# Optimization experiments

Hardware: AMD Instinct MI355X
Metric: run time of the kernel (lower is better)

Reference implementation:

```python
import jax, jax.numpy as jnp
import numpy as np

NQ = 8          # n_qubits
NC = 4          # n_cycles of the angle encoder
PI = np.float32(np.pi)
LAYER_QUBITS = [[0, 1, 2, 3, 4, 5, 6, 7], [1, 3, 5, 7]]  # active qubits per conv layer
FINAL_QUBITS = [3, 7]                                    # active after last pooling
CX = jnp.array([[1, 0, 0, 0], [0, 1, 0, 0], [0, 0, 0, 1], [0, 0, 1, 0]], jnp.complex64)


def apply1(psi, U, q):
    """Apply 1-qubit gate U ((2,2) shared or (B,2,2) batched) on qubit q. psi: (B,2,...,2)."""
    psi = jnp.moveaxis(psi, 1 + q, -1)
    if U.ndim == 3:
        psi = jnp.einsum('bij,b...j->b...i', U, psi)
    else:
        psi = jnp.einsum('ij,...j->...i', U, psi)
    return jnp.moveaxis(psi, -1, 1 + q)


def apply2(psi, U, q0, q1):
    """Apply 2-qubit gate U (4,4) on (q0,q1); q0 is the more-significant wire."""
    psi = jnp.moveaxis(psi, (1 + q0, 1 + q1), (-2, -1))
    sh = psi.shape
    psi = jnp.einsum('ij,...j->...i', U, psi.reshape(sh[:-2] + (4,)))
    return jnp.moveaxis(psi.reshape(sh), (-2, -1), (1 + q0, 1 + q1))


def rz_mat(t):
    return jnp.array([[jnp.exp(-0.5j * t), 0.0], [0.0, jnp.exp(0.5j * t)]]).astype(jnp.complex64)


def ry_mat(t):
    c, s = jnp.cos(t / 2), jnp.sin(t / 2)
    return jnp.array([[c, -s], [s, c]]).astype(jnp.complex64)


def crx_mat(t):
    c = jnp.cos(t / 2).astype(jnp.complex64)
    s = jnp.sin(t / 2).astype(jnp.complex64)
    M = jnp.eye(4, dtype=jnp.complex64)
    return M.at[2, 2].set(c).at[3, 3].set(c).at[2, 3].set(-1j * s).at[3, 2].set(-1j * s)


def u3_mat(t, p, l):
    c, s = jnp.cos(t / 2), jnp.sin(t / 2)
    return jnp.array([[c + 0j, -jnp.exp(1j * l) * s],
                      [jnp.exp(1j * p) * s, jnp.exp(1j * (p + l)) * c]]).astype(jnp.complex64)


def expz(psi, q):
    """<Z_q> = P(q=0) - P(q=1)."""
    p = psi.real ** 2 + psi.imag ** 2
    p = jnp.moveaxis(p, 1 + q, 1).reshape(p.shape[0], 2, -1).sum(-1)
    return p[:, 0] - p[:, 1]


def encode(x):
    """Angle-encoding circuit (circuit_builder): NC cycles of RY(x) + CNOT ring."""
    B = x.shape[0]
    psi = jnp.zeros((B, 2 ** NQ), jnp.complex64).at[:, 0].set(1.0).reshape((B,) + (2,) * NQ)
    for c in range(NC):
        ang = x[:, c * NQ:(c + 1) * NQ]
        cc, ss = jnp.cos(ang / 2), jnp.sin(ang / 2)
        for q in range(NQ):
            U = jnp.stack([jnp.stack([cc[:, q], -ss[:, q]], -1),
                           jnp.stack([ss[:, q], cc[:, q]], -1)], -2).astype(jnp.complex64)
            psi = apply1(psi, U, q)
        for q in range(NQ):
            psi = apply2(psi, CX, q, (q + 1) % NQ)
    return psi


def forward(x, rz_p, ry_p, ry2_p, crx_p, u3_p, u3b_p, W1, b1, W2, b2):
    psi0 = encode(x)
    psi1 = psi0  # deepcopy of encoded state for the second feature map
    for layer in range(2):
        aq = LAYER_QUBITS[layer]
        n = len(aq)
        RZp, RYp, RY2p = rz_mat(rz_p[layer]), ry_mat(ry_p[layer]), ry_mat(ry2_p[layer])
        RZm, RZpl = rz_mat(-PI / 2), rz_mat(PI / 2)
        # circuit 1: ZNOTY-style conv blocks, even pairs then odd pairs
        for parity in (0, 1):
            for i in range(parity, n - 1, 2):
                qc, qt = aq[i], aq[i + 1]
                psi0 = apply1(psi0, RZm, qt)
                psi0 = apply2(psi0, CX, qt, qc)
                psi0 = apply1(psi0, RZp, qc)
                psi0 = apply1(psi0, RYp, qt)
                psi0 = apply2(psi0, CX, qc, qt)
                psi0 = apply1(psi0, RY2p, qt)
                psi0 = apply2(psi0, CX, qt, qc)
                psi0 = apply1(psi0, RZpl, qc)
        remain = [aq[i] for i in range(n) if i % 2 == 1]
        U3a = u3_mat(u3_p[layer, 0], u3_p[layer, 1], u3_p[layer, 2])
        for q in remain:
            psi0 = apply1(psi0, U3a, q)
        # circuit 2: CRX conv blocks, even pairs then odd pairs
        CRXp = crx_mat(crx_p[layer])
        for parity in (0, 1):
            for i in range(parity, n - 1, 2):
                psi1 = apply2(psi1, CRXp, aq[i], aq[i + 1])
        U3b = u3_mat(u3b_p[layer, 0], u3b_p[layer, 1], u3b_p[layer, 2])
        for q in remain:
            psi1 = apply1(psi1, U3b, q)
    xv = jnp.stack([expz(psi0, q) for q in FINAL_QUBITS], 1)  # (B,2)
    yv = jnp.stack([expz(psi1, q) for q in FINAL_QUBITS], 1)  # (B,2)
    feat = jnp.concatenate([xv, yv], 1)                       # (B,4)
    h = jnp.tanh(feat @ W1.T + b1)
    return jax.nn.sigmoid(h @ W2.T + b2)


def setup_inputs() -> dict:
    key = jax.random.key(0)
    ks = jax.random.split(key, 12)
    B = 8192
    return {
        'x': jax.random.normal(ks[0], (B, NC * NQ), jnp.float32),
        'rz_p': jax.random.normal(ks[1], (2,), jnp.float32) * 0.5,
        'ry_p': jax.random.normal(ks[2], (2,), jnp.float32) * 0.5,
        'ry2_p': jax.random.normal(ks[3], (2,), jnp.float32) * 0.5,
        'crx_p': jax.random.normal(ks[4], (2,), jnp.float32) * 0.5,
        'u3_p': jax.random.normal(ks[5], (2, 3), jnp.float32) * 0.5,
        'u3b_p': jax.random.normal(ks[6], (2, 3), jnp.float32) * 0.5,
        'W1': jax.random.normal(ks[7], (15, 4), jnp.float32) * 0.4,
        'b1': jax.random.normal(ks[8], (15,), jnp.float32) * 0.1,
        'W2': jax.random.normal(ks[9], (1, 15), jnp.float32) * 0.25,
        'b2': jax.random.normal(ks[10], (1,), jnp.float32) * 0.1,
    }


def reference(x, rz_p, ry_p, ry2_p, crx_p, u3_p, u3b_p, W1, b1, W2, b2):
    return forward(x, rz_p, ry_p, ry2_p, crx_p, u3_p, u3b_p, W1, b1, W2, b2)
```

## Files before the change

kernel.cpp:

```cpp
#include <hip/hip_runtime.h>

#define DEV __device__ __forceinline__

struct C2 { float r, i; };


template<int P>
DEV void ry_cross(float* pr, float* pi, float gc, float gs, int lane) {
  const float cb = ((lane >> P) & 1) ? gs : -gs;
  #pragma unroll
  for (int s = 0; s < 4; ++s) {
    float br = __shfl_xor(pr[s], 1 << P);
    float bi = __shfl_xor(pi[s], 1 << P);
    pr[s] = gc * pr[s] + cb * br;
    pi[s] = gc * pi[s] + cb * bi;
  }
}

template<int M>
DEV void ry_in(float* pr, float* pi, float gc, float gs) {
  #pragma unroll
  for (int s = 0; s < 4; ++s) if (!(s & M)) {
    const int s1 = s | M;
    float ar = pr[s], ai = pi[s], br = pr[s1], bi = pi[s1];
    pr[s]  = gc * ar - gs * br;  pi[s]  = gc * ai - gs * bi;
    pr[s1] = gs * ar + gc * br;  pi[s1] = gs * ai + gc * bi;
  }
}

template<int PC, int PT>
DEV void cx_cc(float* pr, float* pi, int lane) {
  const bool h = (lane >> PC) & 1;
  #pragma unroll
  for (int s = 0; s < 4; ++s) {
    float tr = __shfl_xor(pr[s], 1 << PT);
    float ti = __shfl_xor(pi[s], 1 << PT);
    pr[s] = h ? tr : pr[s];
    pi[s] = h ? ti : pi[s];
  }
}

template<int PC, int MT>
DEV void cx_ci(float* pr, float* pi, int lane) {
  const bool h = (lane >> PC) & 1;
  #pragma unroll
  for (int s = 0; s < 4; ++s) if (!(s & MT)) {
    const int s1 = s | MT;
    float ar = pr[s], br = pr[s1];
    pr[s] = h ? br : ar;  pr[s1] = h ? ar : br;
    float ai = pi[s], bi = pi[s1];
    pi[s] = h ? bi : ai;  pi[s1] = h ? ai : bi;
  }
}

template<int MC, int MT>
DEV void cx_ii(float* pr, float* pi) {
  #pragma unroll
  for (int s = 0; s < 4; ++s) if ((s & MC) && !(s & MT)) {
    const int s1 = s | MT;
    float t;
    t = pr[s]; pr[s] = pr[s1]; pr[s1] = t;
    t = pi[s]; pi[s] = pi[s1]; pi[s1] = t;
  }
}

template<int MC, int PT>
DEV void cx_ic(float* pr, float* pi) {
  #pragma unroll
  for (int s = 0; s < 4; ++s) if (s & MC) {
    pr[s] = __shfl_xor(pr[s], 1 << PT);
    pi[s] = __shfl_xor(pi[s], 1 << PT);
  }
}


template<int PC, int PT>
DEV void u4_cc(float* pr, float* pi, const float* cw, int lay, int lane) {
  const int r = (((lane >> PC) & 1) << 1) | ((lane >> PT) & 1);
  const int base = (lay * 16 + r * 4) * 2;
  const float w0r = cw[base + (r ^ 0) * 2], w0i = cw[base + (r ^ 0) * 2 + 1];
  const float w1r = cw[base + (r ^ 1) * 2], w1i = cw[base + (r ^ 1) * 2 + 1];
  const float w2r = cw[base + (r ^ 2) * 2], w2i = cw[base + (r ^ 2) * 2 + 1];
  const float w3r = cw[base + (r ^ 3) * 2], w3i = cw[base + (r ^ 3) * 2 + 1];
  #pragma unroll
  for (int s = 0; s < 4; ++s) {
    float ar = pr[s], ai = pi[s];
    float tr = __shfl_xor(ar, 1 << PT),               ti = __shfl_xor(ai, 1 << PT);
    float cr = __shfl_xor(ar, 1 << PC),               ci = __shfl_xor(ai, 1 << PC);
    float ur = __shfl_xor(ar, (1 << PC) | (1 << PT)), ui = __shfl_xor(ai, (1 << PC) | (1 << PT));
    pr[s] = w0r*ar - w0i*ai + w1r*tr - w1i*ti + w2r*cr - w2i*ci + w3r*ur - w3i*ui;
    pi[s] = w0r*ai + w0i*ar + w1r*ti + w1i*tr + w2r*ci + w2i*cr + w3r*ui + w3i*ur;
  }
}

template<int PC, int MT>
DEV void u4_ci(float* pr, float* pi, const float* cw, int lay, int lane) {
  const int bc = (lane >> PC) & 1;
  const int r0 = bc << 1, r1 = r0 | 1;
  const int b0 = (lay * 16 + r0 * 4) * 2;
  const int b1 = (lay * 16 + r1 * 4) * 2;
  const float A0r = cw[b0 + (r0 ^ 0) * 2], A0i = cw[b0 + (r0 ^ 0) * 2 + 1];
  const float A1r = cw[b0 + (r0 ^ 1) * 2], A1i = cw[b0 + (r0 ^ 1) * 2 + 1];
  const float A2r = cw[b0 + (r0 ^ 2) * 2], A2i = cw[b0 + (r0 ^ 2) * 2 + 1];
  const float A3r = cw[b0 + (r0 ^ 3) * 2], A3i = cw[b0 + (r0 ^ 3) * 2 + 1];
  const float B0r = cw[b1 + (r1 ^ 0) * 2], B0i = cw[b1 + (r1 ^ 0) * 2 + 1];
  const float B1r = cw[b1 + (r1 ^ 1) * 2], B1i = cw[b1 + (r1 ^ 1) * 2 + 1];
  const float B2r = cw[b1 + (r1 ^ 2) * 2], B2i = cw[b1 + (r1 ^ 2) * 2 + 1];
  const float B3r = cw[b1 + (r1 ^ 3) * 2], B3i = cw[b1 + (r1 ^ 3) * 2 + 1];
  #pragma unroll
  for (int s = 0; s < 4; ++s) if (!(s & MT)) {
    const int s1 = s | MT;
    float ar = pr[s], ai = pi[s], br = pr[s1], bi = pi[s1];
    float xar = __shfl_xor(ar, 1 << PC), xai = __shfl_xor(ai, 1 << PC);
    float xbr = __shfl_xor(br, 1 << PC), xbi = __shfl_xor(bi, 1 << PC);
    pr[s]  = A0r*ar - A0i*ai + A1r*br - A1i*bi + A2r*xar - A2i*xai + A3r*xbr - A3i*xbi;
    pi[s]  = A0r*ai + A0i*ar + A1r*bi + A1i*br + A2r*xai + A2i*xar + A3r*xbi + A3i*xbr;
    pr[s1] = B0r*br - B0i*bi + B1r*ar - B1i*ai + B2r*xbr - B2i*xbi + B3r*xar - B3i*xai;
    pi[s1] = B0r*bi + B0i*br + B1r*ai + B1i*ar + B2r*xbi + B2i*xbr + B3r*xai + B3i*xar;
  }
}

DEV void u4_ii_full(float* pr, float* pi, const float* cw, int lay) {
  float nr[4], ni[4];
  #pragma unroll
  for (int r = 0; r < 4; ++r) {
    float ar = 0.0f, ai = 0.0f;
    #pragma unroll
    for (int c = 0; c < 4; ++c) {
      float ur = cw[(lay * 16 + r * 4 + c) * 2];
      float ui = cw[(lay * 16 + r * 4 + c) * 2 + 1];
      ar += ur * pr[c] - ui * pi[c];
      ai += ur * pi[c] + ui * pr[c];
    }
    nr[r] = ar; ni[r] = ai;
  }
  #pragma unroll
  for (int r = 0; r < 4; ++r) { pr[r] = nr[r]; pi[r] = ni[r]; }
}


DEV void u3_make(float t, float p, float l, C2* u) {
  float c = __cosf(0.5f * t), s = __sinf(0.5f * t);
  float cp = __cosf(p), sp = __sinf(p);
  float cl = __cosf(l), sl = __sinf(l);
  float cpl = __cosf(p + l), spl = __sinf(p + l);
  u[0] = C2{c, 0.0f};
  u[1] = C2{-cl * s, -sl * s};
  u[2] = C2{cp * s, sp * s};
  u[3] = C2{cpl * c, spl * c};
}

template<int P>
DEV void u3_cross(float* pr, float* pi, const C2* u, int lane) {
  const bool h = (lane >> P) & 1;
  const float car = h ? u[3].r : u[0].r, cai = h ? u[3].i : u[0].i;
  const float cbr = h ? u[2].r : u[1].r, cbi = h ? u[2].i : u[1].i;
  #pragma unroll
  for (int s = 0; s < 4; ++s) {
    float br = __shfl_xor(pr[s], 1 << P);
    float bi = __shfl_xor(pi[s], 1 << P);
    float ar = pr[s], ai = pi[s];
    pr[s] = car*ar - cai*ai + cbr*br - cbi*bi;
    pi[s] = car*ai + cai*ar + cbr*bi + cbi*br;
  }
}

template<int M>
DEV void u3_in(float* pr, float* pi, const C2* u) {
  #pragma unroll
  for (int s = 0; s < 4; ++s) if (!(s & M)) {
    const int s1 = s | M;
    float ar = pr[s], ai = pi[s], br = pr[s1], bi = pi[s1];
    pr[s]  = u[0].r*ar - u[0].i*ai + u[1].r*br - u[1].i*bi;
    pi[s]  = u[0].r*ai + u[0].i*ar + u[1].r*bi + u[1].i*br;
    pr[s1] = u[2].r*ar - u[2].i*ai + u[3].r*br - u[3].i*bi;
    pi[s1] = u[2].r*ai + u[2].i*ar + u[3].r*bi + u[3].i*br;
  }
}


template<int PC, int PT>
DEV void crx_cc(float* pr, float* pi, float c, float s, int lane) {
  const bool h = (lane >> PC) & 1;
  const float cc = h ? c : 1.0f;
  const float ss = h ? s : 0.0f;
  #pragma unroll
  for (int k = 0; k < 4; ++k) {
    float br = __shfl_xor(pr[k], 1 << PT);
    float bi = __shfl_xor(pi[k], 1 << PT);
    float ar = pr[k], ai = pi[k];
    pr[k] = cc * ar + ss * bi;
    pi[k] = cc * ai - ss * br;
  }
}

template<int PC, int MT>
DEV void crx_ci(float* pr, float* pi, float c, float s, int lane) {
  const bool h = (lane >> PC) & 1;
  const float cc = h ? c : 1.0f;
  const float ss = h ? s : 0.0f;
  #pragma unroll
  for (int k = 0; k < 4; ++k) if (!(k & MT)) {
    const int k1 = k | MT;
    float ar = pr[k], ai = pi[k], br = pr[k1], bi = pi[k1];
    pr[k]  = cc * ar + ss * bi;
    pi[k]  = cc * ai - ss * br;
    pr[k1] = cc * br + ss * ai;
    pi[k1] = cc * bi - ss * ar;
  }
}

template<int MC, int MT>
DEV void crx_ii(float* pr, float* pi, float c, float s) {
  #pragma unroll
  for (int k = 0; k < 4; ++k) if ((k & MC) && !(k & MT)) {
    const int k1 = k | MT;
    float ar = pr[k], ai = pi[k], br = pr[k1], bi = pi[k1];
    pr[k]  = c * ar + s * bi;
    pi[k]  = c * ai - s * br;
    pr[k1] = c * br + s * ai;
    pi[k1] = c * bi - s * ar;
  }
}


DEV void expz37(const float* pr, const float* pi, int lane, float& z3, float& z7) {
  float t3 = 0.0f, t7 = 0.0f;
  #pragma unroll
  for (int s = 0; s < 4; ++s) {
    float p = pr[s] * pr[s] + pi[s] * pi[s];
    t3 += p;
    t7 += (s & 1) ? -p : p;
  }
  t3 = ((lane >> 2) & 1) ? -t3 : t3;
  #pragma unroll
  for (int m = 1; m < 64; m <<= 1) {
    t3 += __shfl_xor(t3, m);
    t7 += __shfl_xor(t7, m);
  }
  z3 = t3; z7 = t7;
}


__global__ __launch_bounds__(256, 4)
void qcnn_kernel(const float* __restrict__ x,
                 const float* __restrict__ rz_p, const float* __restrict__ ry_p,
                 const float* __restrict__ ry2_p, const float* __restrict__ crx_p,
                 const float* __restrict__ u3_p, const float* __restrict__ u3b_p,
                 const float* __restrict__ W1, const float* __restrict__ b1,
                 const float* __restrict__ W2, const float* __restrict__ b2,
                 float* __restrict__ out, int B) {
  __shared__ float cw[64];

  const int tid  = threadIdx.x;
  const int lane = tid & 63;
  const int wave = tid >> 6;
  const int elem = blockIdx.x * 4 + wave;
  const int elemc = elem < B ? elem : (B - 1);

  if (tid < 32) {
    const int lay = tid >> 4, e = tid & 15, i4 = e >> 2, j4 = e & 3;
    const int base = tid & 48;
    const float c45 = 0.70710678118654752f;
    float rz = rz_p[lay], ry = ry_p[lay], ry2 = ry2_p[lay];
    float mr = (i4 == j4) ? c45 : 0.0f;
    float mi = (i4 == j4) ? ((i4 & 1) ? -c45 : c45) : 0.0f;
    { int t = (i4 & 1) ? (i4 ^ 2) : i4; int src = base | (t << 2) | j4;
      mr = __shfl(mr, src); mi = __shfl(mi, src); }
    { float cz = __cosf(0.5f * rz), sz = __sinf(0.5f * rz);
      float di = (i4 & 2) ? sz : -sz;
      float nr = cz * mr - di * mi, ni = cz * mi + di * mr; mr = nr; mi = ni; }
    { float cy = __cosf(0.5f * ry), sy = __sinf(0.5f * ry);
      int src = base | ((i4 ^ 1) << 2) | j4;
      float orr = __shfl(mr, src), oii = __shfl(mi, src);
      float sg = (i4 & 1) ? sy : -sy;
      mr = cy * mr + sg * orr; mi = cy * mi + sg * oii; }
    { int t = (i4 & 2) ? (i4 ^ 1) : i4; int src = base | (t << 2) | j4;
      mr = __shfl(mr, src); mi = __shfl(mi, src); }
    { float cy = __cosf(0.5f * ry2), sy = __sinf(0.5f * ry2);
      int src = base | ((i4 ^ 1) << 2) | j4;
      float orr = __shfl(mr, src), oii = __shfl(mi, src);
      float sg = (i4 & 1) ? sy : -sy;
      mr = cy * mr + sg * orr; mi = cy * mi + sg * oii; }
    { int t = (i4 & 1) ? (i4 ^ 2) : i4; int src = base | (t << 2) | j4;
      mr = __shfl(mr, src); mi = __shfl(mi, src); }
    { float di = (i4 & 2) ? c45 : -c45;
      float nr = c45 * mr - di * mi, ni = c45 * mi + di * mr; mr = nr; mi = ni; }
    cw[(lay * 16 + e) * 2]     = mr;
    cw[(lay * 16 + e) * 2 + 1] = mi;
  }

  float a0 = x[(size_t)elemc * 32 + (lane & 31)];
  float ch = __cosf(0.5f * a0), sh = __sinf(0.5f * a0);

  float pr[4], pi[4];
  #pragma unroll
  for (int s = 0; s < 4; ++s) { pr[s] = 0.0f; pi[s] = 0.0f; }
  pr[0] = (lane == 0) ? 1.0f : 0.0f;

  #pragma unroll 1
  for (int c = 0; c < 4; ++c) {
    const int cb = c * 8;
    float gc, gs;
    gc = __shfl(ch, cb + 0); gs = __shfl(sh, cb + 0); ry_cross<5>(pr, pi, gc, gs, lane);
    gc = __shfl(ch, cb + 1); gs = __shfl(sh, cb + 1); ry_cross<4>(pr, pi, gc, gs, lane);
    gc = __shfl(ch, cb + 2); gs = __shfl(sh, cb + 2); ry_cross<3>(pr, pi, gc, gs, lane);
    gc = __shfl(ch, cb + 3); gs = __shfl(sh, cb + 3); ry_cross<2>(pr, pi, gc, gs, lane);
    gc = __shfl(ch, cb + 4); gs = __shfl(sh, cb + 4); ry_cross<1>(pr, pi, gc, gs, lane);
    gc = __shfl(ch, cb + 5); gs = __shfl(sh, cb + 5); ry_cross<0>(pr, pi, gc, gs, lane);
    gc = __shfl(ch, cb + 6); gs = __shfl(sh, cb + 6); ry_in<2>(pr, pi, gc, gs);
    gc = __shfl(ch, cb + 7); gs = __shfl(sh, cb + 7); ry_in<1>(pr, pi, gc, gs);
    cx_cc<5, 4>(pr, pi, lane);
    cx_cc<4, 3>(pr, pi, lane);
    cx_cc<3, 2>(pr, pi, lane);
    cx_cc<2, 1>(pr, pi, lane);
    cx_cc<1, 0>(pr, pi, lane);
    cx_ci<0, 2>(pr, pi, lane);
    cx_ii<2, 1>(pr, pi);
    cx_ic<1, 5>(pr, pi);
  }

  float qr[4], qi[4];
  #pragma unroll
  for (int s = 0; s < 4; ++s) { qr[s] = pr[s]; qi[s] = pi[s]; }

  __syncthreads();

  u4_cc<5, 4>(pr, pi, cw, 0, lane);
  u4_cc<3, 2>(pr, pi, cw, 0, lane);
  u4_cc<1, 0>(pr, pi, cw, 0, lane);
  u4_ii_full(pr, pi, cw, 0);
  u4_cc<4, 3>(pr, pi, cw, 0, lane);
  u4_cc<2, 1>(pr, pi, cw, 0, lane);
  u4_ci<0, 2>(pr, pi, cw, 0, lane);
  {
    C2 u[4]; u3_make(u3_p[0], u3_p[1], u3_p[2], u);
    u3_cross<4>(pr, pi, u, lane);
    u3_cross<2>(pr, pi, u, lane);
    u3_cross<0>(pr, pi, u, lane);
    u3_in<1>(pr, pi, u);
  }
  u4_cc<4, 2>(pr, pi, cw, 1, lane);
  u4_ci<0, 1>(pr, pi, cw, 1, lane);
  u4_cc<2, 0>(pr, pi, cw, 1, lane);
  {
    C2 u[4]; u3_make(u3_p[3], u3_p[4], u3_p[5], u);
    u3_cross<2>(pr, pi, u, lane);
    u3_in<1>(pr, pi, u);
  }

  {
    float t = crx_p[0];
    float cc = __cosf(0.5f * t), ss = __sinf(0.5f * t);
    crx_cc<5, 4>(qr, qi, cc, ss, lane);
    crx_cc<3, 2>(qr, qi, cc, ss, lane);
    crx_cc<1, 0>(qr, qi, cc, ss, lane);
    crx_ii<2, 1>(qr, qi, cc, ss);
    crx_cc<4, 3>(qr, qi, cc, ss, lane);
    crx_cc<2, 1>(qr, qi, cc, ss, lane);
    crx_ci<0, 2>(qr, qi, cc, ss, lane);
  }
  {
    C2 u[4]; u3_make(u3b_p[0], u3b_p[1], u3b_p[2], u);
    u3_cross<4>(qr, qi, u, lane);
    u3_cross<2>(qr, qi, u, lane);
    u3_cross<0>(qr, qi, u, lane);
    u3_in<1>(qr, qi, u);
  }
  {
    float t = crx_p[1];
    float cc = __cosf(0.5f * t), ss = __sinf(0.5f * t);
    crx_cc<4, 2>(qr, qi, cc, ss, lane);
    crx_ci<0, 1>(qr, qi, cc, ss, lane);
    crx_cc<2, 0>(qr, qi, cc, ss, lane);
  }
  {
    C2 u[4]; u3_make(u3b_p[3], u3b_p[4], u3b_p[5], u);
    u3_cross<2>(qr, qi, u, lane);
    u3_in<1>(qr, qi, u);
  }

  float f0, f1, f2, f3;
  expz37(pr, pi, lane, f0, f1);
  expz37(qr, qi, lane, f2, f3);

  const int sub = lane & 15;
  const int j = (sub < 15) ? sub : 0;
  float acc = W1[j * 4 + 0] * f0 + W1[j * 4 + 1] * f1 +
              W1[j * 4 + 2] * f2 + W1[j * 4 + 3] * f3 + b1[j];
  float e2 = __expf(2.0f * acc);
  float th = (e2 - 1.0f) / (e2 + 1.0f);
  float part = (sub < 15) ? th * W2[j] : 0.0f;
  #pragma unroll
  for (int m = 1; m < 16; m <<= 1) part += __shfl_xor(part, m);

  if (lane == 0 && elem < B) {
    float z = part + b2[0];
    out[elem] = 1.0f / (1.0f + __expf(-z));
  }
}

extern "C" void kernel_launch(void* const* d_in, const int* in_sizes, int n_in,
                              void* d_out, int out_size, void* d_ws, size_t ws_size,
                              hipStream_t stream) {
  (void)n_in; (void)out_size; (void)d_ws; (void)ws_size;
  const float* x     = (const float*)d_in[0];
  const float* rz_p  = (const float*)d_in[1];
  const float* ry_p  = (const float*)d_in[2];
  const float* ry2_p = (const float*)d_in[3];
  const float* crx_p = (const float*)d_in[4];
  const float* u3_p  = (const float*)d_in[5];
  const float* u3b_p = (const float*)d_in[6];
  const float* W1    = (const float*)d_in[7];
  const float* b1    = (const float*)d_in[8];
  const float* W2    = (const float*)d_in[9];
  const float* b2    = (const float*)d_in[10];
  float* out = (float*)d_out;

  const int B = in_sizes[0] / 32;
  const int blocks = (B + 3) / 4;
  qcnn_kernel<<<dim3(blocks), dim3(256), 0, stream>>>(
      x, rz_p, ry_p, ry2_p, crx_p, u3_p, u3b_p, W1, b1, W2, b2, out, B);
}
```

Measured before the change: 141.7 us.

## Map two batch elements per wave with 8 amplitudes per lane

Each wave now simulates two batch elements, one per 32-lane half, and each lane holds 8 complex amplitudes in registers instead of 4. The qubit-to-lane and qubit-to-register mapping changes to match, and the two branch circuits (u4/u3 and crx/u3b) are interleaved for more instruction-level parallelism. The aim is to halve the number of waves and turn more gates into register-local work rather than cross-lane shuffles. In exchange each lane uses more registers, which may lower occupancy.

```diff
diff --git a/kernel.cpp b/kernel.cpp
--- a/kernel.cpp
+++ b/kernel.cpp
@@ -9,7 +9,7 @@
 DEV void ry_cross(float* pr, float* pi, float gc, float gs, int lane) {
   const float cb = ((lane >> P) & 1) ? gs : -gs;
   #pragma unroll
-  for (int s = 0; s < 4; ++s) {
+  for (int s = 0; s < 8; ++s) {
     float br = __shfl_xor(pr[s], 1 << P);
     float bi = __shfl_xor(pi[s], 1 << P);
     pr[s] = gc * pr[s] + cb * br;
@@ -20,7 +20,7 @@
 template<int M>
 DEV void ry_in(float* pr, float* pi, float gc, float gs) {
   #pragma unroll
-  for (int s = 0; s < 4; ++s) if (!(s & M)) {
+  for (int s = 0; s < 8; ++s) if (!(s & M)) {
     const int s1 = s | M;
     float ar = pr[s], ai = pi[s], br = pr[s1], bi = pi[s1];
     pr[s]  = gc * ar - gs * br;  pi[s]  = gc * ai - gs * bi;
@@ -32,7 +32,7 @@
 DEV void cx_cc(float* pr, float* pi, int lane) {
   const bool h = (lane >> PC) & 1;
   #pragma unroll
-  for (int s = 0; s < 4; ++s) {
+  for (int s = 0; s < 8; ++s) {
     float tr = __shfl_xor(pr[s], 1 << PT);
     float ti = __shfl_xor(pi[s], 1 << PT);
     pr[s] = h ? tr : pr[s];
@@ -44,7 +44,7 @@
 DEV void cx_ci(float* pr, float* pi, int lane) {
   const bool h = (lane >> PC) & 1;
   #pragma unroll
-  for (int s = 0; s < 4; ++s) if (!(s & MT)) {
+  for (int s = 0; s < 8; ++s) if (!(s & MT)) {
     const int s1 = s | MT;
     float ar = pr[s], br = pr[s1];
     pr[s] = h ? br : ar;  pr[s1] = h ? ar : br;
@@ -56,7 +56,7 @@
 template<int MC, int MT>
 DEV void cx_ii(float* pr, float* pi) {
   #pragma unroll
-  for (int s = 0; s < 4; ++s) if ((s & MC) && !(s & MT)) {
+  for (int s = 0; s < 8; ++s) if ((s & MC) && !(s & MT)) {
     const int s1 = s | MT;
     float t;
     t = pr[s]; pr[s] = pr[s1]; pr[s1] = t;
@@ -67,7 +67,7 @@
 template<int MC, int PT>
 DEV void cx_ic(float* pr, float* pi) {
   #pragma unroll
-  for (int s = 0; s < 4; ++s) if (s & MC) {
+  for (int s = 0; s < 8; ++s) if (s & MC) {
     pr[s] = __shfl_xor(pr[s], 1 << PT);
     pi[s] = __shfl_xor(pi[s], 1 << PT);
   }
@@ -83,7 +83,7 @@
   const float w2r = cw[base + (r ^ 2) * 2], w2i = cw[base + (r ^ 2) * 2 + 1];
   const float w3r = cw[base + (r ^ 3) * 2], w3i = cw[base + (r ^ 3) * 2 + 1];
   #pragma unroll
-  for (int s = 0; s < 4; ++s) {
+  for (int s = 0; s < 8; ++s) {
     float ar = pr[s], ai = pi[s];
     float tr = __shfl_xor(ar, 1 << PT),               ti = __shfl_xor(ai, 1 << PT);
     float cr = __shfl_xor(ar, 1 << PC),               ci = __shfl_xor(ai, 1 << PC);
@@ -108,7 +108,7 @@
   const float B2r = cw[b1 + (r1 ^ 2) * 2], B2i = cw[b1 + (r1 ^ 2) * 2 + 1];
   const float B3r = cw[b1 + (r1 ^ 3) * 2], B3i = cw[b1 + (r1 ^ 3) * 2 + 1];
   #pragma unroll
-  for (int s = 0; s < 4; ++s) if (!(s & MT)) {
+  for (int s = 0; s < 8; ++s) if (!(s & MT)) {
     const int s1 = s | MT;
     float ar = pr[s], ai = pi[s], br = pr[s1], bi = pi[s1];
     float xar = __shfl_xor(ar, 1 << PC), xai = __shfl_xor(ai, 1 << PC);
@@ -120,22 +120,25 @@
   }
 }
 
-DEV void u4_ii_full(float* pr, float* pi, const float* cw, int lay) {
-  float nr[4], ni[4];
-  #pragma unroll
-  for (int r = 0; r < 4; ++r) {
-    float ar = 0.0f, ai = 0.0f;
-    #pragma unroll
-    for (int c = 0; c < 4; ++c) {
-      float ur = cw[(lay * 16 + r * 4 + c) * 2];
-      float ui = cw[(lay * 16 + r * 4 + c) * 2 + 1];
-      ar += ur * pr[c] - ui * pi[c];
-      ai += ur * pi[c] + ui * pr[c];
-    }
-    nr[r] = ar; ni[r] = ai;
-  }
-  #pragma unroll
-  for (int r = 0; r < 4; ++r) { pr[r] = nr[r]; pi[r] = ni[r]; }
+template<int MC, int MT>
+DEV void u4_ii(float* pr, float* pi, const float* cw, int lay) {
+  #pragma unroll
+  for (int s = 0; s < 8; ++s) if (!(s & (MC | MT))) {
+    const int s0 = s, s1 = s | MT, s2 = s | MC, s3 = s | MC | MT;
+    float v0r = pr[s0], v0i = pi[s0], v1r = pr[s1], v1i = pi[s1];
+    float v2r = pr[s2], v2i = pi[s2], v3r = pr[s3], v3i = pi[s3];
+    const float* u = cw + lay * 32;
+    float n0r = u[0]*v0r - u[1]*v0i + u[2]*v1r - u[3]*v1i + u[4]*v2r - u[5]*v2i + u[6]*v3r - u[7]*v3i;
+    float n0i = u[0]*v0i + u[1]*v0r + u[2]*v1i + u[3]*v1r + u[4]*v2i + u[5]*v2r + u[6]*v3i + u[7]*v3r;
+    float n1r = u[8]*v0r - u[9]*v0i + u[10]*v1r - u[11]*v1i + u[12]*v2r - u[13]*v2i + u[14]*v3r - u[15]*v3i;
+    float n1i = u[8]*v0i + u[9]*v0r + u[10]*v1i + u[11]*v1r + u[12]*v2i + u[13]*v2r + u[14]*v3i + u[15]*v3r;
+    float n2r = u[16]*v0r - u[17]*v0i + u[18]*v1r - u[19]*v1i + u[20]*v2r - u[21]*v2i + u[22]*v3r - u[23]*v3i;
+    float n2i = u[16]*v0i + u[17]*v0r + u[18]*v1i + u[19]*v1r + u[20]*v2i + u[21]*v2r + u[22]*v3i + u[23]*v3r;
+    float n3r = u[24]*v0r - u[25]*v0i + u[26]*v1r - u[27]*v1i + u[28]*v2r - u[29]*v2i + u[30]*v3r - u[31]*v3i;
+    float n3i = u[24]*v0i + u[25]*v0r + u[26]*v1i + u[27]*v1r + u[28]*v2i + u[29]*v2r + u[30]*v3i + u[31]*v3r;
+    pr[s0] = n0r; pi[s0] = n0i; pr[s1] = n1r; pi[s1] = n1i;
+    pr[s2] = n2r; pi[s2] = n2i; pr[s3] = n3r; pi[s3] = n3i;
+  }
 }
 
 
@@ -156,7 +159,7 @@
   const float car = h ? u[3].r : u[0].r, cai = h ? u[3].i : u[0].i;
   const float cbr = h ? u[2].r : u[1].r, cbi = h ? u[2].i : u[1].i;
   #pragma unroll
-  for (int s = 0; s < 4; ++s) {
+  for (int s = 0; s < 8; ++s) {
     float br = __shfl_xor(pr[s], 1 << P);
     float bi = __shfl_xor(pi[s], 1 << P);
     float ar = pr[s], ai = pi[s];
@@ -168,7 +171,7 @@
 template<int M>
 DEV void u3_in(float* pr, float* pi, const C2* u) {
   #pragma unroll
-  for (int s = 0; s < 4; ++s) if (!(s & M)) {
+  for (int s = 0; s < 8; ++s) if (!(s & M)) {
     const int s1 = s | M;
     float ar = pr[s], ai = pi[s], br = pr[s1], bi = pi[s1];
     pr[s]  = u[0].r*ar - u[0].i*ai + u[1].r*br - u[1].i*bi;
@@ -185,7 +188,7 @@
   const float cc = h ? c : 1.0f;
   const float ss = h ? s : 0.0f;
   #pragma unroll
-  for (int k = 0; k < 4; ++k) {
+  for (int k = 0; k < 8; ++k) {
     float br = __shfl_xor(pr[k], 1 << PT);
     float bi = __shfl_xor(pi[k], 1 << PT);
     float ar = pr[k], ai = pi[k];
@@ -200,7 +203,7 @@
   const float cc = h ? c : 1.0f;
   const float ss = h ? s : 0.0f;
   #pragma unroll
-  for (int k = 0; k < 4; ++k) if (!(k & MT)) {
+  for (int k = 0; k < 8; ++k) if (!(k & MT)) {
     const int k1 = k | MT;
     float ar = pr[k], ai = pi[k], br = pr[k1], bi = pi[k1];
     pr[k]  = cc * ar + ss * bi;
@@ -213,7 +216,7 @@
 template<int MC, int MT>
 DEV void crx_ii(float* pr, float* pi, float c, float s) {
   #pragma unroll
-  for (int k = 0; k < 4; ++k) if ((k & MC) && !(k & MT)) {
+  for (int k = 0; k < 8; ++k) if ((k & MC) && !(k & MT)) {
     const int k1 = k | MT;
     float ar = pr[k], ai = pi[k], br = pr[k1], bi = pi[k1];
     pr[k]  = c * ar + s * bi;
@@ -227,14 +230,14 @@
 DEV void expz37(const float* pr, const float* pi, int lane, float& z3, float& z7) {
   float t3 = 0.0f, t7 = 0.0f;
   #pragma unroll
-  for (int s = 0; s < 4; ++s) {
+  for (int s = 0; s < 8; ++s) {
     float p = pr[s] * pr[s] + pi[s] * pi[s];
     t3 += p;
     t7 += (s & 1) ? -p : p;
   }
-  t3 = ((lane >> 2) & 1) ? -t3 : t3;
-  #pragma unroll
-  for (int m = 1; m < 64; m <<= 1) {
+  t3 = ((lane >> 1) & 1) ? -t3 : t3;
+  #pragma unroll
+  for (int m = 1; m < 32; m <<= 1) {
     t3 += __shfl_xor(t3, m);
     t7 += __shfl_xor(t7, m);
   }
@@ -255,7 +258,9 @@
   const int tid  = threadIdx.x;
   const int lane = tid & 63;
   const int wave = tid >> 6;
-  const int elem = blockIdx.x * 4 + wave;
+  const int half = lane >> 5;
+  const int l    = lane & 31;
+  const int elem = blockIdx.x * 8 + wave * 2 + half;
   const int elemc = elem < B ? elem : (B - 1);
 
   if (tid < 32) {
@@ -290,111 +295,87 @@
     cw[(lay * 16 + e) * 2 + 1] = mi;
   }
 
-  float a0 = x[(size_t)elemc * 32 + (lane & 31)];
+  float a0 = x[(size_t)elemc * 32 + l];
   float ch = __cosf(0.5f * a0), sh = __sinf(0.5f * a0);
 
-  float pr[4], pi[4];
-  #pragma unroll
-  for (int s = 0; s < 4; ++s) { pr[s] = 0.0f; pi[s] = 0.0f; }
-  pr[0] = (lane == 0) ? 1.0f : 0.0f;
-
+  float pr[8], pi[8];
+  #pragma unroll
+  for (int s = 0; s < 8; ++s) { pr[s] = 0.0f; pi[s] = 0.0f; }
+  pr[0] = (l == 0) ? 1.0f : 0.0f;
+
+  const int hb = lane & 32;
   #pragma unroll 1
   for (int c = 0; c < 4; ++c) {
     const int cb = c * 8;
     float gc, gs;
-    gc = __shfl(ch, cb + 0); gs = __shfl(sh, cb + 0); ry_cross<5>(pr, pi, gc, gs, lane);
-    gc = __shfl(ch, cb + 1); gs = __shfl(sh, cb + 1); ry_cross<4>(pr, pi, gc, gs, lane);
-    gc = __shfl(ch, cb + 2); gs = __shfl(sh, cb + 2); ry_cross<3>(pr, pi, gc, gs, lane);
-    gc = __shfl(ch, cb + 3); gs = __shfl(sh, cb + 3); ry_cross<2>(pr, pi, gc, gs, lane);
-    gc = __shfl(ch, cb + 4); gs = __shfl(sh, cb + 4); ry_cross<1>(pr, pi, gc, gs, lane);
-    gc = __shfl(ch, cb + 5); gs = __shfl(sh, cb + 5); ry_cross<0>(pr, pi, gc, gs, lane);
-    gc = __shfl(ch, cb + 6); gs = __shfl(sh, cb + 6); ry_in<2>(pr, pi, gc, gs);
-    gc = __shfl(ch, cb + 7); gs = __shfl(sh, cb + 7); ry_in<1>(pr, pi, gc, gs);
-    cx_cc<5, 4>(pr, pi, lane);
+    gc = __shfl(ch, hb | (cb + 0)); gs = __shfl(sh, hb | (cb + 0)); ry_cross<4>(pr, pi, gc, gs, lane);
+    gc = __shfl(ch, hb | (cb + 1)); gs = __shfl(sh, hb | (cb + 1)); ry_cross<3>(pr, pi, gc, gs, lane);
+    gc = __shfl(ch, hb | (cb + 2)); gs = __shfl(sh, hb | (cb + 2)); ry_cross<2>(pr, pi, gc, gs, lane);
+    gc = __shfl(ch, hb | (cb + 3)); gs = __shfl(sh, hb | (cb + 3)); ry_cross<1>(pr, pi, gc, gs, lane);
+    gc = __shfl(ch, hb | (cb + 4)); gs = __shfl(sh, hb | (cb + 4)); ry_cross<0>(pr, pi, gc, gs, lane);
+    gc = __shfl(ch, hb | (cb + 5)); gs = __shfl(sh, hb | (cb + 5)); ry_in<4>(pr, pi, gc, gs);
+    gc = __shfl(ch, hb | (cb + 6)); gs = __shfl(sh, hb | (cb + 6)); ry_in<2>(pr, pi, gc, gs);
+    gc = __shfl(ch, hb | (cb + 7)); gs = __shfl(sh, hb | (cb + 7)); ry_in<1>(pr, pi, gc, gs);
     cx_cc<4, 3>(pr, pi, lane);
     cx_cc<3, 2>(pr, pi, lane);
     cx_cc<2, 1>(pr, pi, lane);
     cx_cc<1, 0>(pr, pi, lane);
-    cx_ci<0, 2>(pr, pi, lane);
+    cx_ci<0, 4>(pr, pi, lane);
+    cx_ii<4, 2>(pr, pi);
     cx_ii<2, 1>(pr, pi);
-    cx_ic<1, 5>(pr, pi);
-  }
-
-  float qr[4], qi[4];
-  #pragma unroll
-  for (int s = 0; s < 4; ++s) { qr[s] = pr[s]; qi[s] = pi[s]; }
+    cx_ic<1, 4>(pr, pi);
+  }
+
+  float qr[8], qi[8];
+  #pragma unroll
+  for (int s = 0; s < 8; ++s) { qr[s] = pr[s]; qi[s] = pi[s]; }
 
   __syncthreads();
 
-  u4_cc<5, 4>(pr, pi, cw, 0, lane);
-  u4_cc<3, 2>(pr, pi, cw, 0, lane);
-  u4_cc<1, 0>(pr, pi, cw, 0, lane);
-  u4_ii_full(pr, pi, cw, 0);
-  u4_cc<4, 3>(pr, pi, cw, 0, lane);
-  u4_cc<2, 1>(pr, pi, cw, 0, lane);
-  u4_ci<0, 2>(pr, pi, cw, 0, lane);
+  float cc0, ss0, cc1, ss1;
+  { float t = crx_p[0]; cc0 = __cosf(0.5f * t); ss0 = __sinf(0.5f * t); }
+  { float t = crx_p[1]; cc1 = __cosf(0.5f * t); ss1 = __sinf(0.5f * t); }
+
+  u4_cc<4, 3>(pr, pi, cw, 0, lane);   crx_cc<4, 3>(qr, qi, cc0, ss0, lane);
+  u4_cc<2, 1>(pr, pi, cw, 0, lane);   crx_cc<2, 1>(qr, qi, cc0, ss0, lane);
+  u4_ci<0, 4>(pr, pi, cw, 0, lane);   crx_ci<0, 4>(qr, qi, cc0, ss0, lane);
+  u4_ii<2, 1>(pr, pi, cw, 0);         crx_ii<2, 1>(qr, qi, cc0, ss0);
+  u4_cc<3, 2>(pr, pi, cw, 0, lane);   crx_cc<3, 2>(qr, qi, cc0, ss0, lane);
+  u4_cc<1, 0>(pr, pi, cw, 0, lane);   crx_cc<1, 0>(qr, qi, cc0, ss0, lane);
+  u4_ii<4, 2>(pr, pi, cw, 0);         crx_ii<4, 2>(qr, qi, cc0, ss0);
   {
-    C2 u[4]; u3_make(u3_p[0], u3_p[1], u3_p[2], u);
-    u3_cross<4>(pr, pi, u, lane);
-    u3_cross<2>(pr, pi, u, lane);
-    u3_cross<0>(pr, pi, u, lane);
-    u3_in<1>(pr, pi, u);
-  }
-  u4_cc<4, 2>(pr, pi, cw, 1, lane);
-  u4_ci<0, 1>(pr, pi, cw, 1, lane);
-  u4_cc<2, 0>(pr, pi, cw, 1, lane);
+    C2 ua[4]; u3_make(u3_p[0], u3_p[1], u3_p[2], ua);
+    C2 ub[4]; u3_make(u3b_p[0], u3b_p[1], u3b_p[2], ub);
+    u3_cross<3>(pr, pi, ua, lane);    u3_cross<3>(qr, qi, ub, lane);
+    u3_cross<1>(pr, pi, ua, lane);    u3_cross<1>(qr, qi, ub, lane);
+    u3_in<4>(pr, pi, ua);             u3_in<4>(qr, qi, ub);
+    u3_in<1>(pr, pi, ua);             u3_in<1>(qr, qi, ub);
+  }
+
+  u4_cc<3, 1>(pr, pi, cw, 1, lane);   crx_cc<3, 1>(qr, qi, cc1, ss1, lane);
+  u4_ii<4, 1>(pr, pi, cw, 1);         crx_ii<4, 1>(qr, qi, cc1, ss1);
+  u4_ci<1, 4>(pr, pi, cw, 1, lane);   crx_ci<1, 4>(qr, qi, cc1, ss1, lane);
   {
-    C2 u[4]; u3_make(u3_p[3], u3_p[4], u3_p[5], u);
-    u3_cross<2>(pr, pi, u, lane);
-    u3_in<1>(pr, pi, u);
-  }
-
-  {
-    float t = crx_p[0];
-    float cc = __cosf(0.5f * t), ss = __sinf(0.5f * t);
-    crx_cc<5, 4>(qr, qi, cc, ss, lane);
-    crx_cc<3, 2>(qr, qi, cc, ss, lane);
-    crx_cc<1, 0>(qr, qi, cc, ss, lane);
-    crx_ii<2, 1>(qr, qi, cc, ss);
-    crx_cc<4, 3>(qr, qi, cc, ss, lane);
-    crx_cc<2, 1>(qr, qi, cc, ss, lane);
-    crx_ci<0, 2>(qr, qi, cc, ss, lane);
-  }
-  {
-    C2 u[4]; u3_make(u3b_p[0], u3b_p[1], u3b_p[2], u);
-    u3_cross<4>(qr, qi, u, lane);
-    u3_cross<2>(qr, qi, u, lane);
-    u3_cross<0>(qr, qi, u, lane);
-    u3_in<1>(qr, qi, u);
-  }
-  {
-    float t = crx_p[1];
-    float cc = __cosf(0.5f * t), ss = __sinf(0.5f * t);
-    crx_cc<4, 2>(qr, qi, cc, ss, lane);
-    crx_ci<0, 1>(qr, qi, cc, ss, lane);
-    crx_cc<2, 0>(qr, qi, cc, ss, lane);
-  }
-  {
-    C2 u[4]; u3_make(u3b_p[3], u3b_p[4], u3b_p[5], u);
-    u3_cross<2>(qr, qi, u, lane);
-    u3_in<1>(qr, qi, u);
+    C2 ua[4]; u3_make(u3_p[3], u3_p[4], u3_p[5], ua);
+    C2 ub[4]; u3_make(u3b_p[3], u3b_p[4], u3b_p[5], ub);
+    u3_cross<1>(pr, pi, ua, lane);    u3_cross<1>(qr, qi, ub, lane);
+    u3_in<1>(pr, pi, ua);             u3_in<1>(qr, qi, ub);
   }
 
   float f0, f1, f2, f3;
   expz37(pr, pi, lane, f0, f1);
   expz37(qr, qi, lane, f2, f3);
 
-  const int sub = lane & 15;
-  const int j = (sub < 15) ? sub : 0;
+  const int j = (l < 15) ? l : 0;
   float acc = W1[j * 4 + 0] * f0 + W1[j * 4 + 1] * f1 +
               W1[j * 4 + 2] * f2 + W1[j * 4 + 3] * f3 + b1[j];
   float e2 = __expf(2.0f * acc);
   float th = (e2 - 1.0f) / (e2 + 1.0f);
-  float part = (sub < 15) ? th * W2[j] : 0.0f;
+  float part = (l < 15) ? th * W2[j] : 0.0f;
   #pragma unroll
   for (int m = 1; m < 16; m <<= 1) part += __shfl_xor(part, m);
 
-  if (lane == 0 && elem < B) {
+  if (l == 0 && elem < B) {
     float z = part + b2[0];
     out[elem] = 1.0f / (1.0f + __expf(-z));
   }
@@ -418,7 +399,7 @@
   float* out = (float*)d_out;
 
   const int B = in_sizes[0] / 32;
-  const int blocks = (B + 3) / 4;
+  const int blocks = (B + 7) / 8;
   qcnn_kernel<<<dim3(blocks), dim3(256), 0, stream>>>(
       x, rz_p, ry_p, ry2_p, crx_p, u3_p, u3b_p, W1, b1, W2, b2, out, B);
 }
```

New measurement: 141.7 us. About the same (-0.0%).
